# Kernel tuning notes

Hardware: AMD Instinct MI355X
Metric: run time of the kernel (lower is better)

## Reference

```python
import jax, jax.numpy as jnp
import numpy as np

B, L, H = 32, 2048, 512


def setup_inputs() -> dict:
    key = jax.random.key(0)
    k1, k2, k3, k4, k5, k6 = jax.random.split(key, 6)
    scale = 1.0 / np.sqrt(H)
    return {
        "query": jax.random.normal(k1, (B, H), dtype=jnp.float32),
        "ref": jax.random.normal(k2, (B, L, H), dtype=jnp.float32),
        "mask": jax.random.randint(k3, (B, L), 0, 2) == 1,
        # learned params (torch Linear weight layout: [out, in]; apply as x @ W.T)
        "W_ref": jax.random.normal(k4, (H, H), dtype=jnp.float32) * scale,
        "W_q": jax.random.normal(k5, (H, H), dtype=jnp.float32) * scale,
        "v": jax.random.normal(k6, (H,), dtype=jnp.float32) * scale,
    }


def reference(query, ref, mask, W_ref, W_q, v):
    scale = 1.0 / np.sqrt(H)
    # additive (Bahdanau) scores: v^T tanh(W_ref ref + W_q q)
    encoded_ref = jnp.einsum("blh,oh->blo", ref, W_ref)          # (B, L, H)
    encoded_q = jnp.einsum("bh,oh->bo", query, W_q)[:, None, :]  # (B, 1, H)
    scores = jnp.einsum("blh,h->bl", jnp.tanh(encoded_ref + encoded_q), v)
    scores = scores * scale
    scores = jnp.where(mask, -1e9, scores)
    attn = jax.nn.softmax(scores, axis=1)                         # (B, L)
    glimpse = jnp.einsum("bl,blh->bh", attn, ref)                 # (B, H)
    return glimpse, scores
```

## Files before the change

kernel.cpp:

```cpp
#include <hip/hip_runtime.h>
#include <hip/hip_bf16.h>
#include <cstdint>

typedef __attribute__((ext_vector_type(4))) float f32x4;
typedef __attribute__((ext_vector_type(8))) short s16x8;

#define NB   32
#define NL   2048
#define NH   512
#define NM   (NB * NL)
#define SCALE 0.04419417382415922f

__device__ __forceinline__ ushort f2bf(float f) {
    __hip_bfloat16 b = __float2bfloat16(f);
    return *reinterpret_cast<ushort*>(&b);
}
__device__ __forceinline__ float bf2f(unsigned u) {
    union { unsigned u; float f; } a; a.u = u << 16; return a.f;
}

__device__ __forceinline__ void gl16(const ushort* g, ushort* l) {
    __builtin_amdgcn_global_load_lds(
        (const __attribute__((address_space(1))) unsigned int*)g,
        (__attribute__((address_space(3))) unsigned int*)l,
        16, 0, 0);
}

__global__ __launch_bounds__(256) void k_convW(const float* __restrict__ W,
                                               ushort* __restrict__ Wb) {
    int i = blockIdx.x * 256 + threadIdx.x;
    const float4* s = (const float4*)W;
    float4 a = s[2 * i], c = s[2 * i + 1];
    union { ushort u[8]; int4 v; } p;
    p.u[0] = f2bf(a.x); p.u[1] = f2bf(a.y); p.u[2] = f2bf(a.z); p.u[3] = f2bf(a.w);
    p.u[4] = f2bf(c.x); p.u[5] = f2bf(c.y); p.u[6] = f2bf(c.z); p.u[7] = f2bf(c.w);
    ((int4*)Wb)[i] = p.v;
}

__global__ __launch_bounds__(256) void k_convRef(const float* __restrict__ ref,
                                                 ushort* __restrict__ refb) {
    int i = blockIdx.x * 256 + threadIdx.x;
    const float4* s = (const float4*)ref;
#pragma unroll
    for (int it = 0; it < 8; ++it) {
        int idx = it * 4194304 / 8 * 2;
        int ci = i + it * 524288;
        float4 a = s[2 * ci], c = s[2 * ci + 1];
        union { ushort u[8]; int4 v; } p;
        p.u[0] = f2bf(a.x); p.u[1] = f2bf(a.y); p.u[2] = f2bf(a.z); p.u[3] = f2bf(a.w);
        p.u[4] = f2bf(c.x); p.u[5] = f2bf(c.y); p.u[6] = f2bf(c.z); p.u[7] = f2bf(c.w);
        ((int4*)refb)[ci] = p.v;
        (void)idx;
    }
}

__global__ __launch_bounds__(512) void k_eq(const float* __restrict__ query,
                                            const float* __restrict__ Wq,
                                            float* __restrict__ eq) {
    int b = blockIdx.x;
    int o = threadIdx.x;
    __shared__ float q[NH];
    q[o] = query[b * NH + o];
    __syncthreads();
    const float4* w = (const float4*)(Wq + (size_t)o * NH);
    float acc = 0.f;
#pragma unroll 4
    for (int i = 0; i < NH / 4; ++i) {
        float4 x = w[i];
        acc += q[4 * i] * x.x + q[4 * i + 1] * x.y + q[4 * i + 2] * x.z + q[4 * i + 3] * x.w;
    }
    eq[b * NH + o] = acc;
}

__global__ __launch_bounds__(256) void k_gemm_bf(const ushort* __restrict__ refb,
                                                 const ushort* __restrict__ Wb,
                                                 const float* __restrict__ eq,
                                                 const float* __restrict__ v,
                                                 float* __restrict__ part) {
    __shared__ ushort As[2][128 * 32];
    __shared__ ushort Bs[2][128 * 32];

    int tid = threadIdx.x;
    int lane = tid & 63, wid = tid >> 6;
    int wr = wid >> 1, wc = wid & 1;

    int phys = blockIdx.x;
    int xcd = phys & 7, slot = phys >> 3;
    int mt = xcd * 64 + (slot >> 2);
    int nt = slot & 3;
    int m0 = mt * 128, n0 = nt * 128;
    int b = mt >> 4;

    f32x4 acc[4][4];
#pragma unroll
    for (int i = 0; i < 4; ++i)
#pragma unroll
        for (int j = 0; j < 4; ++j) acc[i][j] = (f32x4)(0.f);

    int cc = wid * 2;
    int grow = lane >> 2, gcol = (lane & 3) * 8;
    const ushort* aglob = refb + (size_t)(m0 + cc * 16 + grow) * NH + gcol;
    const ushort* bglob = Wb + (size_t)(n0 + cc * 16 + grow) * NH + gcol;

    int lr = lane & 15, kq = lane >> 4;
    int aoff[4], boff[4];
#pragma unroll
    for (int f = 0; f < 4; ++f) {
        aoff[f] = (wr * 64 + f * 16 + lr) * 32 + kq * 8;
        boff[f] = (wc * 64 + f * 16 + lr) * 32 + kq * 8;
    }

#define STAGE(buf, kt)                                      \
    {   gl16(aglob + (kt) * 32, &As[buf][cc * 512]);        \
        gl16(aglob + (kt) * 32 + 16 * NH, &As[buf][(cc + 1) * 512]); \
        gl16(bglob + (kt) * 32, &Bs[buf][cc * 512]);        \
        gl16(bglob + (kt) * 32 + 16 * NH, &Bs[buf][(cc + 1) * 512]); }

#define READ_FRAGS(buf)                                     \
    _Pragma("unroll")                                       \
    for (int f = 0; f < 4; ++f) af[f] = *(const s16x8*)&As[buf][aoff[f]]; \
    _Pragma("unroll")                                       \
    for (int f = 0; f < 4; ++f) bfr[f] = *(const s16x8*)&Bs[buf][boff[f]];

#define DO_MFMA()                                           \
    _Pragma("unroll")                                       \
    for (int fr = 0; fr < 4; ++fr)                          \
        _Pragma("unroll")                                   \
        for (int fc = 0; fc < 4; ++fc)                      \
            acc[fr][fc] = __builtin_amdgcn_mfma_f32_16x16x32_bf16(af[fr], bfr[fc], acc[fr][fc], 0, 0, 0);

    STAGE(0, 0)
    __syncthreads();

    for (int t2 = 0; t2 < 8; ++t2) {
        s16x8 af[4], bfr[4];
        int k0 = 2 * t2;
        if (k0 + 1 < 16) STAGE(1, k0 + 1)
        READ_FRAGS(0)
        DO_MFMA()
        __syncthreads();
        if (k0 + 2 < 16) STAGE(0, k0 + 2)
        READ_FRAGS(1)
        DO_MFMA()
        __syncthreads();
    }
#undef STAGE
#undef READ_FRAGS
#undef DO_MFMA

    const float* eqb = eq + b * NH;
    float vv[4], ee[4];
#pragma unroll
    for (int fc = 0; fc < 4; ++fc) {
        int c = n0 + wc * 64 + fc * 16 + lr;
        vv[fc] = v[c];
        ee[fc] = eqb[c];
    }
#pragma unroll
    for (int fr = 0; fr < 4; ++fr) {
#pragma unroll
        for (int reg = 0; reg < 4; ++reg) {
            float s = 0.f;
#pragma unroll
            for (int fc = 0; fc < 4; ++fc) {
                float x = acc[fr][fc][reg] + ee[fc];
                float t = 1.f - 2.f / (__expf(2.f * x) + 1.f);
                s += vv[fc] * t;
            }
            s += __shfl_xor(s, 1);
            s += __shfl_xor(s, 2);
            s += __shfl_xor(s, 4);
            s += __shfl_xor(s, 8);
            if (lr == 0) {
                int row = wr * 64 + fr * 16 + kq * 4 + reg;
                part[(size_t)nt * NM + m0 + row] = s;
            }
        }
    }
}

#define LDST 36
__global__ __launch_bounds__(256) void k_gemm_f32(const float* __restrict__ ref,
                                                  const ushort* __restrict__ Wb,
                                                  const float* __restrict__ eq,
                                                  const float* __restrict__ v,
                                                  float* __restrict__ part) {
    __shared__ ushort As[128 * LDST];
    __shared__ ushort Bs[128 * LDST];
    int tid = threadIdx.x;
    int lane = tid & 63, wid = tid >> 6;
    int wr = wid >> 1, wc = wid & 1;
    int phys = blockIdx.x;
    int xcd = phys & 7, slot = phys >> 3;
    int mt = xcd * 64 + (slot >> 2);
    int nt = slot & 3;
    int m0 = mt * 128, n0 = nt * 128;
    int b = mt >> 4;
    f32x4 acc[4][4];
#pragma unroll
    for (int i = 0; i < 4; ++i)
#pragma unroll
        for (int j = 0; j < 4; ++j) acc[i][j] = (f32x4)(0.f);
    int srow = tid >> 1, sks = (tid & 1) * 16;
    const float*  asrc = ref + (size_t)(m0 + srow) * NH + sks;
    const ushort* bsrc = Wb + (size_t)(n0 + srow) * NH + sks;
    int awr = srow * LDST + sks;
    int lr = lane & 15, kq = lane >> 4;
    int aoff[4], boff[4];
#pragma unroll
    for (int f = 0; f < 4; ++f) {
        aoff[f] = (wr * 64 + f * 16 + lr) * LDST + kq * 8;
        boff[f] = (wc * 64 + f * 16 + lr) * LDST + kq * 8;
    }
    float4 pa0, pa1, pa2, pa3;
    int4 pb0, pb1;
    {
        const float* s = asrc;
        pa0 = *(const float4*)(s); pa1 = *(const float4*)(s + 4);
        pa2 = *(const float4*)(s + 8); pa3 = *(const float4*)(s + 12);
        const int4* bs = (const int4*)(bsrc);
        pb0 = bs[0]; pb1 = bs[1];
    }
    for (int kt = 0; kt < 16; ++kt) {
        union { ushort u[8]; int4 v; } p0, p1;
        p0.u[0] = f2bf(pa0.x); p0.u[1] = f2bf(pa0.y); p0.u[2] = f2bf(pa0.z); p0.u[3] = f2bf(pa0.w);
        p0.u[4] = f2bf(pa1.x); p0.u[5] = f2bf(pa1.y); p0.u[6] = f2bf(pa1.z); p0.u[7] = f2bf(pa1.w);
        p1.u[0] = f2bf(pa2.x); p1.u[1] = f2bf(pa2.y); p1.u[2] = f2bf(pa2.z); p1.u[3] = f2bf(pa2.w);
        p1.u[4] = f2bf(pa3.x); p1.u[5] = f2bf(pa3.y); p1.u[6] = f2bf(pa3.z); p1.u[7] = f2bf(pa3.w);
        *(int4*)&As[awr] = p0.v; *(int4*)&As[awr + 8] = p1.v;
        *(int4*)&Bs[awr] = pb0;  *(int4*)&Bs[awr + 8] = pb1;
        __syncthreads();
        if (kt < 15) {
            const float* s = asrc + (kt + 1) * 32;
            pa0 = *(const float4*)(s); pa1 = *(const float4*)(s + 4);
            pa2 = *(const float4*)(s + 8); pa3 = *(const float4*)(s + 12);
            const int4* bs = (const int4*)(bsrc + (kt + 1) * 32);
            pb0 = bs[0]; pb1 = bs[1];
        }
        s16x8 af[4], bfr[4];
#pragma unroll
        for (int f = 0; f < 4; ++f) af[f] = *(const s16x8*)&As[aoff[f]];
#pragma unroll
        for (int f = 0; f < 4; ++f) bfr[f] = *(const s16x8*)&Bs[boff[f]];
        __syncthreads();
#pragma unroll
        for (int fr = 0; fr < 4; ++fr)
#pragma unroll
            for (int fc = 0; fc < 4; ++fc)
                acc[fr][fc] = __builtin_amdgcn_mfma_f32_16x16x32_bf16(af[fr], bfr[fc], acc[fr][fc], 0, 0, 0);
    }
    const float* eqb = eq + b * NH;
    float vv[4], ee[4];
#pragma unroll
    for (int fc = 0; fc < 4; ++fc) {
        int c = n0 + wc * 64 + fc * 16 + lr;
        vv[fc] = v[c]; ee[fc] = eqb[c];
    }
#pragma unroll
    for (int fr = 0; fr < 4; ++fr) {
#pragma unroll
        for (int reg = 0; reg < 4; ++reg) {
            float s = 0.f;
#pragma unroll
            for (int fc = 0; fc < 4; ++fc) {
                float x = acc[fr][fc][reg] + ee[fc];
                float t = 1.f - 2.f / (__expf(2.f * x) + 1.f);
                s += vv[fc] * t;
            }
            s += __shfl_xor(s, 1); s += __shfl_xor(s, 2);
            s += __shfl_xor(s, 4); s += __shfl_xor(s, 8);
            if (lr == 0) {
                int row = wr * 64 + fr * 16 + kq * 4 + reg;
                part[(size_t)nt * NM + m0 + row] = s;
            }
        }
    }
}

__global__ __launch_bounds__(256) void k_softmax(const float* __restrict__ part,
                                                 const int* __restrict__ mask,
                                                 float* __restrict__ out_sc,
                                                 float* __restrict__ attn) {
    int b = blockIdx.x;
    int tid = threadIdx.x;
    int lane = tid & 63, wid = tid >> 6;
    __shared__ float red[4];
    float sc[8];
    float mx = -3.4e38f;
#pragma unroll
    for (int i = 0; i < 8; ++i) {
        int m = b * NL + i * 256 + tid;
        float s = (part[m] + part[NM + m] + part[2 * NM + m] + part[3 * NM + m]) * SCALE;
        if (mask[m] != 0) s = -1e9f;
        out_sc[m] = s;
        sc[i] = s;
        mx = fmaxf(mx, s);
    }
#pragma unroll
    for (int o = 32; o >= 1; o >>= 1) mx = fmaxf(mx, __shfl_xor(mx, o));
    if (lane == 0) red[wid] = mx;
    __syncthreads();
    mx = fmaxf(fmaxf(red[0], red[1]), fmaxf(red[2], red[3]));
    __syncthreads();
    float ls = 0.f;
#pragma unroll
    for (int i = 0; i < 8; ++i) {
        float e = __expf(sc[i] - mx);
        sc[i] = e;
        ls += e;
    }
#pragma unroll
    for (int o = 32; o >= 1; o >>= 1) ls += __shfl_xor(ls, o);
    if (lane == 0) red[wid] = ls;
    __syncthreads();
    float inv = 1.f / (red[0] + red[1] + red[2] + red[3]);
#pragma unroll
    for (int i = 0; i < 8; ++i) attn[b * NL + i * 256 + tid] = sc[i] * inv;
}

__global__ __launch_bounds__(256) void k_glp_bf(const ushort* __restrict__ refb,
                                                const float* __restrict__ attn,
                                                float* __restrict__ glp) {
    int sp = blockIdx.x, b = blockIdx.y;
    int tid = threadIdx.x;
    const float* attb = attn + b * NL + sp * 128;
    float2 acc = make_float2(0.f, 0.f);
#pragma unroll 4
    for (int l = 0; l < 128; ++l) {
        float a = attb[l];
        unsigned r = ((const unsigned*)(refb + (size_t)(b * NL + sp * 128 + l) * NH))[tid];
        acc.x += a * bf2f(r & 0xFFFFu);
        acc.y += a * bf2f(r >> 16);
    }
    ((float2*)(glp + (size_t)(sp * NB + b) * NH))[tid] = acc;
}

__global__ __launch_bounds__(256) void k_glp_f32(const float* __restrict__ ref,
                                                 const float* __restrict__ attn,
                                                 float* __restrict__ glp) {
    int sp = blockIdx.x, b = blockIdx.y;
    int tid = threadIdx.x;
    const float* attb = attn + b * NL + sp * 128;
    float2 acc = make_float2(0.f, 0.f);
#pragma unroll 4
    for (int l = 0; l < 128; ++l) {
        float a = attb[l];
        const float2* row = (const float2*)(ref + (size_t)(b * NL + sp * 128 + l) * NH);
        float2 r = row[tid];
        acc.x += a * r.x;
        acc.y += a * r.y;
    }
    ((float2*)(glp + (size_t)(sp * NB + b) * NH))[tid] = acc;
}

__global__ __launch_bounds__(256) void k_gred(const float* __restrict__ glp,
                                              float* __restrict__ out_gl) {
    int idx = blockIdx.x * 256 + threadIdx.x;
    float s = 0.f;
#pragma unroll
    for (int sp = 0; sp < 16; ++sp) s += glp[sp * (NB * NH) + idx];
    out_gl[idx] = s;
}

extern "C" void kernel_launch(void* const* d_in, const int* in_sizes, int n_in,
                              void* d_out, int out_size, void* d_ws, size_t ws_size,
                              hipStream_t stream) {
    const float* query = (const float*)d_in[0];
    const float* ref   = (const float*)d_in[1];
    const int*   mask  = (const int*)d_in[2];
    const float* W_ref = (const float*)d_in[3];
    const float* W_q   = (const float*)d_in[4];
    const float* v     = (const float*)d_in[5];

    float* out_gl = (float*)d_out;
    float* out_sc = out_gl + NB * NH;

    char* w = (char*)d_ws;
    ushort* wW  = (ushort*)w;

    if (ws_size >= (size_t)70100000) {
        ushort* refb = (ushort*)(w + 524288);
        float* eq    = (float*)(w + 524288 + 67108864);
        float* part  = (float*)(w + 524288 + 67108864 + 65536);
        float* attn  = (float*)(w + 524288 + 67108864 + 65536 + 1048576);
        float* glp   = (float*)(w + 524288 + 67108864 + 65536 + 1048576 + 262144);

        k_convW<<<128, 256, 0, stream>>>(W_ref, wW);
        k_convRef<<<2048, 256, 0, stream>>>(ref, refb);
        k_eq<<<NB, 512, 0, stream>>>(query, W_q, eq);
        k_gemm_bf<<<2048, 256, 0, stream>>>(refb, wW, eq, v, part);
        k_softmax<<<NB, 256, 0, stream>>>(part, mask, out_sc, attn);
        k_glp_bf<<<dim3(16, NB), 256, 0, stream>>>(refb, attn, glp);
        k_gred<<<64, 256, 0, stream>>>(glp, out_gl);
    } else {
        float* eq   = (float*)(w + 524288);
        float* part = (float*)(w + 589824);
        float* attn = (float*)(w + 1638400);
        float* glp  = (float*)(w + 1900544);

        k_convW<<<128, 256, 0, stream>>>(W_ref, wW);
        k_eq<<<NB, 512, 0, stream>>>(query, W_q, eq);
        k_gemm_f32<<<2048, 256, 0, stream>>>(ref, wW, eq, v, part);
        k_softmax<<<NB, 256, 0, stream>>>(part, mask, out_sc, attn);
        k_glp_f32<<<dim3(16, NB), 256, 0, stream>>>(ref, attn, glp);
        k_gred<<<64, 256, 0, stream>>>(glp, out_gl);
    }
}
```

Measured before the change: 145.9 us.

## Merge prep kernels and fuse softmax with glimpse reduction

Combines the W conversion, ref conversion and query projection into one multi-role prep kernel, which removes two launches. Softmax is fused into the glimpse kernel: each of 8 sequence-split blocks per batch recomputes the full max and sum from the partial scores, then applies its own slice of exp weights to the bf16 ref rows. This drops the attn buffer round trip and one launch. The cost is redundant softmax work (8x reads of part and mask), fewer glimpse blocks (256 instead of 512) with longer loops, and the GEMM gets a min-blocks-per-CU launch bound hint of 3.

```diff
diff --git a/kernel.cpp b/kernel.cpp
--- a/kernel.cpp
+++ b/kernel.cpp
@@ -26,57 +26,61 @@
         16, 0, 0);
 }
 
-__global__ __launch_bounds__(256) void k_convW(const float* __restrict__ W,
-                                               ushort* __restrict__ Wb) {
-    int i = blockIdx.x * 256 + threadIdx.x;
-    const float4* s = (const float4*)W;
-    float4 a = s[2 * i], c = s[2 * i + 1];
-    union { ushort u[8]; int4 v; } p;
-    p.u[0] = f2bf(a.x); p.u[1] = f2bf(a.y); p.u[2] = f2bf(a.z); p.u[3] = f2bf(a.w);
-    p.u[4] = f2bf(c.x); p.u[5] = f2bf(c.y); p.u[6] = f2bf(c.z); p.u[7] = f2bf(c.w);
-    ((int4*)Wb)[i] = p.v;
-}
-
-__global__ __launch_bounds__(256) void k_convRef(const float* __restrict__ ref,
-                                                 ushort* __restrict__ refb) {
-    int i = blockIdx.x * 256 + threadIdx.x;
-    const float4* s = (const float4*)ref;
-#pragma unroll
-    for (int it = 0; it < 8; ++it) {
-        int idx = it * 4194304 / 8 * 2;
-        int ci = i + it * 524288;
-        float4 a = s[2 * ci], c = s[2 * ci + 1];
+__global__ __launch_bounds__(256) void k_prep(const float* __restrict__ ref,
+                                              ushort* __restrict__ refb,
+                                              const float* __restrict__ W,
+                                              ushort* __restrict__ Wb,
+                                              const float* __restrict__ query,
+                                              const float* __restrict__ Wq,
+                                              float* __restrict__ eq) {
+    int bid = blockIdx.x;
+    if (bid < 2048) {
+        int i = bid * 256 + threadIdx.x;
+        const float4* s = (const float4*)ref;
+#pragma unroll
+        for (int it = 0; it < 8; ++it) {
+            int ci = i + it * 524288;
+            float4 a = s[2 * ci], c = s[2 * ci + 1];
+            union { ushort u[8]; int4 v; } p;
+            p.u[0] = f2bf(a.x); p.u[1] = f2bf(a.y); p.u[2] = f2bf(a.z); p.u[3] = f2bf(a.w);
+            p.u[4] = f2bf(c.x); p.u[5] = f2bf(c.y); p.u[6] = f2bf(c.z); p.u[7] = f2bf(c.w);
+            ((int4*)refb)[ci] = p.v;
+        }
+    } else if (bid < 2176) {
+        int i = (bid - 2048) * 256 + threadIdx.x;
+        const float4* s = (const float4*)W;
+        float4 a = s[2 * i], c = s[2 * i + 1];
         union { ushort u[8]; int4 v; } p;
         p.u[0] = f2bf(a.x); p.u[1] = f2bf(a.y); p.u[2] = f2bf(a.z); p.u[3] = f2bf(a.w);
         p.u[4] = f2bf(c.x); p.u[5] = f2bf(c.y); p.u[6] = f2bf(c.z); p.u[7] = f2bf(c.w);
-        ((int4*)refb)[ci] = p.v;
-        (void)idx;
-    }
-}
-
-__global__ __launch_bounds__(512) void k_eq(const float* __restrict__ query,
-                                            const float* __restrict__ Wq,
-                                            float* __restrict__ eq) {
-    int b = blockIdx.x;
-    int o = threadIdx.x;
-    __shared__ float q[NH];
-    q[o] = query[b * NH + o];
-    __syncthreads();
-    const float4* w = (const float4*)(Wq + (size_t)o * NH);
-    float acc = 0.f;
+        ((int4*)Wb)[i] = p.v;
+    } else {
+        __shared__ float q[NH];
+        int b = bid - 2176;
+        int t = threadIdx.x;
+        q[t] = query[b * NH + t];
+        q[t + 256] = query[b * NH + t + 256];
+        __syncthreads();
+#pragma unroll
+        for (int half = 0; half < 2; ++half) {
+            int o = t + half * 256;
+            const float4* w = (const float4*)(Wq + (size_t)o * NH);
+            float acc = 0.f;
 #pragma unroll 4
-    for (int i = 0; i < NH / 4; ++i) {
-        float4 x = w[i];
-        acc += q[4 * i] * x.x + q[4 * i + 1] * x.y + q[4 * i + 2] * x.z + q[4 * i + 3] * x.w;
-    }
-    eq[b * NH + o] = acc;
-}
-
-__global__ __launch_bounds__(256) void k_gemm_bf(const ushort* __restrict__ refb,
-                                                 const ushort* __restrict__ Wb,
-                                                 const float* __restrict__ eq,
-                                                 const float* __restrict__ v,
-                                                 float* __restrict__ part) {
+            for (int i = 0; i < NH / 4; ++i) {
+                float4 x = w[i];
+                acc += q[4 * i] * x.x + q[4 * i + 1] * x.y + q[4 * i + 2] * x.z + q[4 * i + 3] * x.w;
+            }
+            eq[b * NH + o] = acc;
+        }
+    }
+}
+
+__global__ __launch_bounds__(256, 3) void k_gemm_bf(const ushort* __restrict__ refb,
+                                                    const ushort* __restrict__ Wb,
+                                                    const float* __restrict__ eq,
+                                                    const float* __restrict__ v,
+                                                    float* __restrict__ part) {
     __shared__ ushort As[2][128 * 32];
     __shared__ ushort Bs[2][128 * 32];
 
@@ -179,7 +183,97 @@
     }
 }
 
+__global__ __launch_bounds__(256) void k_smglp(const float* __restrict__ part,
+                                               const int* __restrict__ mask,
+                                               const ushort* __restrict__ refb,
+                                               float* __restrict__ out_sc,
+                                               float* __restrict__ glp) {
+    int sp = blockIdx.x, b = blockIdx.y;
+    int tid = threadIdx.x;
+    int lane = tid & 63, wid = tid >> 6;
+    __shared__ float red[4];
+    __shared__ float asl[256];
+    float sc[8];
+    float mx = -3.4e38f;
+#pragma unroll
+    for (int i = 0; i < 8; ++i) {
+        int m = b * NL + i * 256 + tid;
+        float s = (part[m] + part[NM + m] + part[2 * NM + m] + part[3 * NM + m]) * SCALE;
+        if (mask[m] != 0) s = -1e9f;
+        if (sp == 0) out_sc[m] = s;
+        sc[i] = s;
+        mx = fmaxf(mx, s);
+    }
+#pragma unroll
+    for (int o = 32; o >= 1; o >>= 1) mx = fmaxf(mx, __shfl_xor(mx, o));
+    if (lane == 0) red[wid] = mx;
+    __syncthreads();
+    mx = fmaxf(fmaxf(red[0], red[1]), fmaxf(red[2], red[3]));
+    __syncthreads();
+    float ls = 0.f;
+#pragma unroll
+    for (int i = 0; i < 8; ++i) {
+        float e = __expf(sc[i] - mx);
+        ls += e;
+        if (i == sp) asl[tid] = e;
+    }
+#pragma unroll
+    for (int o = 32; o >= 1; o >>= 1) ls += __shfl_xor(ls, o);
+    if (lane == 0) red[wid] = ls;
+    __syncthreads();
+    float inv = 1.f / (red[0] + red[1] + red[2] + red[3]);
+
+    const ushort* rb = refb + ((size_t)b * NL + sp * 256) * NH;
+    float2 acc = make_float2(0.f, 0.f);
+#pragma unroll 4
+    for (int l = 0; l < 256; ++l) {
+        float a = asl[l];
+        unsigned r = ((const unsigned*)(rb + (size_t)l * NH))[tid];
+        acc.x += a * bf2f(r & 0xFFFFu);
+        acc.y += a * bf2f(r >> 16);
+    }
+    acc.x *= inv;
+    acc.y *= inv;
+    ((float2*)(glp + (size_t)(sp * NB + b) * NH))[tid] = acc;
+}
+
+__global__ __launch_bounds__(256) void k_gred(const float* __restrict__ glp,
+                                              float* __restrict__ out_gl) {
+    int idx = blockIdx.x * 256 + threadIdx.x;
+    float s = 0.f;
+#pragma unroll
+    for (int sp = 0; sp < 8; ++sp) s += glp[sp * (NB * NH) + idx];
+    out_gl[idx] = s;
+}
+
 #define LDST 36
+__global__ __launch_bounds__(256) void k_convW_f(const float* __restrict__ W,
+                                                 ushort* __restrict__ Wb) {
+    int i = blockIdx.x * 256 + threadIdx.x;
+    const float4* s = (const float4*)W;
+    float4 a = s[2 * i], c = s[2 * i + 1];
+    union { ushort u[8]; int4 v; } p;
+    p.u[0] = f2bf(a.x); p.u[1] = f2bf(a.y); p.u[2] = f2bf(a.z); p.u[3] = f2bf(a.w);
+    p.u[4] = f2bf(c.x); p.u[5] = f2bf(c.y); p.u[6] = f2bf(c.z); p.u[7] = f2bf(c.w);
+    ((int4*)Wb)[i] = p.v;
+}
+__global__ __launch_bounds__(512) void k_eq_f(const float* __restrict__ query,
+                                              const float* __restrict__ Wq,
+                                              float* __restrict__ eq) {
+    int b = blockIdx.x;
+    int o = threadIdx.x;
+    __shared__ float q[NH];
+    q[o] = query[b * NH + o];
+    __syncthreads();
+    const float4* w = (const float4*)(Wq + (size_t)o * NH);
+    float acc = 0.f;
+#pragma unroll 4
+    for (int i = 0; i < NH / 4; ++i) {
+        float4 x = w[i];
+        acc += q[4 * i] * x.x + q[4 * i + 1] * x.y + q[4 * i + 2] * x.z + q[4 * i + 3] * x.w;
+    }
+    eq[b * NH + o] = acc;
+}
 __global__ __launch_bounds__(256) void k_gemm_f32(const float* __restrict__ ref,
                                                   const ushort* __restrict__ Wb,
                                                   const float* __restrict__ eq,
@@ -276,11 +370,10 @@
         }
     }
 }
-
-__global__ __launch_bounds__(256) void k_softmax(const float* __restrict__ part,
-                                                 const int* __restrict__ mask,
-                                                 float* __restrict__ out_sc,
-                                                 float* __restrict__ attn) {
+__global__ __launch_bounds__(256) void k_softmax_f(const float* __restrict__ part,
+                                                   const int* __restrict__ mask,
+                                                   float* __restrict__ out_sc,
+                                                   float* __restrict__ attn) {
     int b = blockIdx.x;
     int tid = threadIdx.x;
     int lane = tid & 63, wid = tid >> 6;
@@ -317,24 +410,6 @@
 #pragma unroll
     for (int i = 0; i < 8; ++i) attn[b * NL + i * 256 + tid] = sc[i] * inv;
 }
-
-__global__ __launch_bounds__(256) void k_glp_bf(const ushort* __restrict__ refb,
-                                                const float* __restrict__ attn,
-                                                float* __restrict__ glp) {
-    int sp = blockIdx.x, b = blockIdx.y;
-    int tid = threadIdx.x;
-    const float* attb = attn + b * NL + sp * 128;
-    float2 acc = make_float2(0.f, 0.f);
-#pragma unroll 4
-    for (int l = 0; l < 128; ++l) {
-        float a = attb[l];
-        unsigned r = ((const unsigned*)(refb + (size_t)(b * NL + sp * 128 + l) * NH))[tid];
-        acc.x += a * bf2f(r & 0xFFFFu);
-        acc.y += a * bf2f(r >> 16);
-    }
-    ((float2*)(glp + (size_t)(sp * NB + b) * NH))[tid] = acc;
-}
-
 __global__ __launch_bounds__(256) void k_glp_f32(const float* __restrict__ ref,
                                                  const float* __restrict__ attn,
                                                  float* __restrict__ glp) {
@@ -352,9 +427,8 @@
     }
     ((float2*)(glp + (size_t)(sp * NB + b) * NH))[tid] = acc;
 }
-
-__global__ __launch_bounds__(256) void k_gred(const float* __restrict__ glp,
-                                              float* __restrict__ out_gl) {
+__global__ __launch_bounds__(256) void k_gred16(const float* __restrict__ glp,
+                                                float* __restrict__ out_gl) {
     int idx = blockIdx.x * 256 + threadIdx.x;
     float s = 0.f;
 #pragma unroll
@@ -382,15 +456,11 @@
         ushort* refb = (ushort*)(w + 524288);
         float* eq    = (float*)(w + 524288 + 67108864);
         float* part  = (float*)(w + 524288 + 67108864 + 65536);
-        float* attn  = (float*)(w + 524288 + 67108864 + 65536 + 1048576);
-        float* glp   = (float*)(w + 524288 + 67108864 + 65536 + 1048576 + 262144);
-
-        k_convW<<<128, 256, 0, stream>>>(W_ref, wW);
-        k_convRef<<<2048, 256, 0, stream>>>(ref, refb);
-        k_eq<<<NB, 512, 0, stream>>>(query, W_q, eq);
+        float* glp   = (float*)(w + 524288 + 67108864 + 65536 + 1048576);
+
+        k_prep<<<2208, 256, 0, stream>>>(ref, refb, W_ref, wW, query, W_q, eq);
         k_gemm_bf<<<2048, 256, 0, stream>>>(refb, wW, eq, v, part);
-        k_softmax<<<NB, 256, 0, stream>>>(part, mask, out_sc, attn);
-        k_glp_bf<<<dim3(16, NB), 256, 0, stream>>>(refb, attn, glp);
+        k_smglp<<<dim3(8, NB), 256, 0, stream>>>(part, mask, refb, out_sc, glp);
         k_gred<<<64, 256, 0, stream>>>(glp, out_gl);
     } else {
         float* eq   = (float*)(w + 524288);
@@ -398,11 +468,11 @@
         float* attn = (float*)(w + 1638400);
         float* glp  = (float*)(w + 1900544);
 
-        k_convW<<<128, 256, 0, stream>>>(W_ref, wW);
-        k_eq<<<NB, 512, 0, stream>>>(query, W_q, eq);
+        k_convW_f<<<128, 256, 0, stream>>>(W_ref, wW);
+        k_eq_f<<<NB, 512, 0, stream>>>(query, W_q, eq);
         k_gemm_f32<<<2048, 256, 0, stream>>>(ref, wW, eq, v, part);
-        k_softmax<<<NB, 256, 0, stream>>>(part, mask, out_sc, attn);
+        k_softmax_f<<<NB, 256, 0, stream>>>(part, mask, out_sc, attn);
         k_glp_f32<<<dim3(16, NB), 256, 0, stream>>>(ref, attn, glp);
-        k_gred<<<64, 256, 0, stream>>>(glp, out_gl);
-    }
-}
+        k_gred16<<<64, 256, 0, stream>>>(glp, out_gl);
+    }
+}
```

Measured after the change: 142.6 us. 2.3% less time.
